# Kernel tuning notes

Hardware: AMD Instinct MI355X
Metric: run time of the kernel (lower is better)

The kernel has to match this reference:

```python
import jax, jax.numpy as jnp
import numpy as np

NSAMPLE = 3  # three_nn default
EPS = 1e-10
CLAMP = 10.0


def setup_inputs() -> dict:
    key = jax.random.key(0)
    k1, k2, k3 = jax.random.split(key, 3)
    B, C, N = 4, 3, 8192
    pos1 = jax.random.normal(k1, (B, C, N), dtype=jnp.float32)
    pos2 = jax.random.normal(k2, (B, C, N), dtype=jnp.float32)
    flow1 = jax.random.normal(k3, (B, C, N), dtype=jnp.float32) * 0.1
    return {"pos1": pos1, "pos2": pos2, "flow1": flow1}


def reference(pos1, pos2, flow1):
    # pos1, flow1: [B,3,N1]; pos2: [B,3,N2]
    pos1_to_2 = pos1 + flow1                       # warped source points [B,3,N1]
    q = jnp.transpose(pos2, (0, 2, 1))             # queries  [B,N2,3]
    k = jnp.transpose(pos1_to_2, (0, 2, 1))        # database [B,N1,3]

    # brute-force 3-NN: squared distances [B,N2,N1]
    d2 = (jnp.sum(q * q, axis=-1, keepdims=True)
          - 2.0 * jnp.einsum('bqc,bnc->bqn', q, k)
          + jnp.sum(k * k, axis=-1)[:, None, :])
    _, knn_idx = jax.lax.top_k(-d2, NSAMPLE)       # [B,N2,NSAMPLE] into N1

    # gather neighbor coords: [B,N2,NSAMPLE,3]
    grouped_pts = jax.vmap(lambda pts, ii: pts[ii])(k, knn_idx)
    diff = grouped_pts - q[:, :, None, :]
    dist = jnp.maximum(jnp.linalg.norm(diff, axis=-1), EPS)  # [B,N2,NSAMPLE]
    inv = 1.0 / dist
    weight = inv / jnp.sum(inv, axis=-1, keepdims=True)      # [B,N2,NSAMPLE]

    # gather neighbor flows and do inverse-distance-weighted average
    flow_t = jnp.transpose(flow1, (0, 2, 1))                 # [B,N1,3]
    grouped_flow = jax.vmap(lambda f, ii: f[ii])(flow_t, knn_idx)  # [B,N2,NSAMPLE,3]
    flow2 = jnp.sum(weight[..., None] * grouped_flow, axis=2)      # [B,N2,3]

    warped = pos2 - jnp.transpose(flow2, (0, 2, 1))          # [B,3,N2]
    return jnp.clip(warped, -CLAMP, CLAMP)
```

## Files before the change

### kernel.cpp

```cpp
#include <hip/hip_runtime.h>
#include <math.h>


#define BB 4
#define NN 8192
#define BBNN (BB * NN)
#define NC 30
#define NCELLS (NC * NC * NC)
#define NCT (BB * NCELLS)
#define GRID_R 3.3f
#define GRID_INVH (1.0f / 0.22f)
#define D3_THR (0.44f * 0.44f * 0.999f)
#define EPB 1024
#define SB 106
#define NZ4 ((NCT + 108 + 4) / 4)
#define ST_PART 0x40000000u
#define ST_DONE 0x80000000u
#define ST_VAL 0x3FFFFFFFu

typedef unsigned long long u64;

__device__ __forceinline__ int cell_of(float x) {
  int c = (int)floorf((x + GRID_R) * GRID_INVH);
  return min(max(c, 0), NC - 1);
}

__device__ __forceinline__ void merge3(u64& a0, u64& a1, u64& a2,
                                       u64 b0, u64 b1, u64 b2) {
  const u64 lo0 = a0 < b0 ? a0 : b0;
  const u64 hi0 = a0 < b0 ? b0 : a0;
  const u64 lo1 = a1 < b1 ? a1 : b1;
  const u64 lo2 = a2 < b2 ? a2 : b2;
  const u64 o1 = hi0 < lo1 ? hi0 : lo1;
  const u64 t = hi0 < lo1 ? lo1 : hi0;
  a0 = lo0;
  a1 = o1;
  a2 = t < lo2 ? t : lo2;
}

__device__ __forceinline__ void insert3(u64& s0, u64& s1, u64& s2, u64 key) {
  const bool c0 = key < s0;
  const bool c1 = key < s1;
  const bool c2 = key < s2;
  s2 = c1 ? s1 : (c2 ? key : s2);
  s1 = c0 ? s0 : (c1 ? key : s1);
  s0 = c0 ? key : s0;
}

__device__ __forceinline__ void wave_merge3(u64& s0, u64& s1, u64& s2) {
#pragma unroll
  for (int mask = 32; mask >= 1; mask >>= 1) {
    const u64 b0 = __shfl_xor(s0, mask, 64);
    const u64 b1 = __shfl_xor(s1, mask, 64);
    const u64 b2 = __shfl_xor(s2, mask, 64);
    merge3(s0, s1, s2, b0, b1, b2);
  }
}

__device__ __forceinline__ void cand1(const float4& a, float qx, float qy,
                                      float qz, u64& s0, u64& s1, u64& s2) {
  const float dx = a.x - qx, dy = a.y - qy, dz = a.z - qz;
  const float d2 = fmaf(dx, dx, fmaf(dy, dy, dz * dz));
  insert3(s0, s1, s2,
          ((u64)__float_as_uint(d2) << 32) | (unsigned)__float_as_uint(a.w));
}

__device__ __forceinline__ void idw_out(int b, int qn, float qx, float qy,
                                        float qz, u64 s0, u64 s1, u64 s2,
                                        const float* __restrict__ P1,
                                        const float* __restrict__ F1,
                                        float* __restrict__ out) {
  const int idxs[3] = {(int)(unsigned)s0 & (NN - 1),
                       (int)(unsigned)s1 & (NN - 1),
                       (int)(unsigned)s2 & (NN - 1)};
  float w[3], gfx[3], gfy[3], gfz[3];
  float wsumv = 0.0f;
#pragma unroll
  for (int r = 0; r < 3; ++r) {
    const int idx = idxs[r];
    const float fx = F1[idx], fy = F1[NN + idx], fz = F1[2 * NN + idx];
    const float kx = P1[idx] + fx;
    const float ky = P1[NN + idx] + fy;
    const float kz = P1[2 * NN + idx] + fz;
    const float dx = kx - qx, dy = ky - qy, dz = kz - qz;
    float d = sqrtf(dx * dx + dy * dy + dz * dz);
    d = fmaxf(d, 1e-10f);
    const float inv = 1.0f / d;
    w[r] = inv; wsumv += inv;
    gfx[r] = fx; gfy[r] = fy; gfz[r] = fz;
  }
  const float invw = 1.0f / wsumv;
  float ox = 0.0f, oy = 0.0f, oz = 0.0f;
#pragma unroll
  for (int r = 0; r < 3; ++r) {
    const float ww = w[r] * invw;
    ox = fmaf(ww, gfx[r], ox);
    oy = fmaf(ww, gfy[r], oy);
    oz = fmaf(ww, gfz[r], oz);
  }
  ox = qx - ox; oy = qy - oy; oz = qz - oz;
  ox = fminf(fmaxf(ox, -10.0f), 10.0f);
  oy = fminf(fmaxf(oy, -10.0f), 10.0f);
  oz = fminf(fmaxf(oz, -10.0f), 10.0f);
  float* o = out + (size_t)b * 3 * NN;
  o[qn] = ox;
  o[NN + qn] = oy;
  o[2 * NN + qn] = oz;
}

__global__ __launch_bounds__(256) void k_zero(int4* __restrict__ p) {
  const int i = blockIdx.x * 256 + threadIdx.x;
  if (i < NZ4) p[i] = make_int4(0, 0, 0, 0);
}

__global__ __launch_bounds__(256) void k_count(const float* __restrict__ p1,
                                               const float* __restrict__ f1,
                                               int* __restrict__ counts) {
  const int gid = blockIdx.x * 256 + threadIdx.x;
  const int b = gid >> 13, n = gid & (NN - 1);
  const float* P = p1 + (size_t)b * 3 * NN;
  const float* F = f1 + (size_t)b * 3 * NN;
  const float x = P[n] + F[n];
  const float y = P[NN + n] + F[NN + n];
  const float z = P[2 * NN + n] + F[2 * NN + n];
  const int cid = (cell_of(z) * NC + cell_of(y)) * NC + cell_of(x);
  atomicAdd(&counts[b * NCELLS + cid], 1);
}

__global__ __launch_bounds__(256) void k_scan(int* __restrict__ counts,
                                              int* __restrict__ offs,
                                              unsigned* __restrict__ scanst) {
  __shared__ int wsums[4];
  __shared__ int sbase;
  const int tid = threadIdx.x, lane = tid & 63, wav = tid >> 6;
  const int bid = blockIdx.x;
  const int c = bid * EPB + tid * 4;
  int4 v = make_int4(0, 0, 0, 0);
  if (c < NCT) {
    v = *reinterpret_cast<const int4*>(counts + c);
    *reinterpret_cast<int4*>(counts + c) = make_int4(0, 0, 0, 0);
  }
  const int sum4 = v.x + v.y + v.z + v.w;
  int incl = sum4;
  for (int off = 1; off < 64; off <<= 1) {
    const int t = __shfl_up(incl, off, 64);
    incl += (lane >= off) ? t : 0;
  }
  if (lane == 63) wsums[wav] = incl;
  __syncthreads();
  int wbase = 0;
#pragma unroll
  for (int w = 0; w < 4; ++w) wbase += (w < wav) ? wsums[w] : 0;
  const int btot = wsums[0] + wsums[1] + wsums[2] + wsums[3];

  if (wav == 0) {
    if (lane == 0) atomicExch(&scanst[bid], ST_PART | (unsigned)btot);
    int base = 0;
    int j0 = bid;
    while (j0 > 0) {
      const int j = j0 - 64 + lane;
      unsigned s;
      if (j >= 0) {
        do { s = atomicAdd(&scanst[j], 0u); } while (s == 0u);
      } else {
        s = ST_DONE;
      }
      const u64 dball = __ballot((s & ST_DONE) != 0);
      int val;
      if (dball) {
        const int hi = 63 - __clzll(dball);
        val = (lane >= hi) ? (int)(s & ST_VAL) : 0;
      } else {
        val = (int)(s & ST_VAL);
      }
      for (int off = 32; off >= 1; off >>= 1) val += __shfl_down(val, off, 64);
      base += __shfl(val, 0, 64);
      if (dball) break;
      j0 -= 64;
    }
    if (lane == 0) {
      atomicExch(&scanst[bid], ST_DONE | (unsigned)(base + btot));
      sbase = base;
    }
  }
  __syncthreads();
  const int excl = sbase + wbase + incl - sum4;
  if (c < NCT) {
    int4 e;
    e.x = excl;
    e.y = excl + v.x;
    e.z = e.y + v.y;
    e.w = e.z + v.z;
    *reinterpret_cast<int4*>(offs + c) = e;
  }
  if (bid == SB - 1 && tid == 0) offs[NCT] = BBNN;
}

__global__ __launch_bounds__(256) void k_scat(const float* __restrict__ p1,
                                              const float* __restrict__ f1,
                                              int* __restrict__ counts,
                                              const int* __restrict__ offs,
                                              float4* __restrict__ csr) {
  const int gid = blockIdx.x * 256 + threadIdx.x;
  const int b = gid >> 13, n = gid & (NN - 1);
  const float* P = p1 + (size_t)b * 3 * NN;
  const float* F = f1 + (size_t)b * 3 * NN;
  const float x = P[n] + F[n];
  const float y = P[NN + n] + F[NN + n];
  const float z = P[2 * NN + n] + F[2 * NN + n];
  const int cid = (cell_of(z) * NC + cell_of(y)) * NC + cell_of(x);
  const int g = b * NCELLS + cid;
  const int rank = atomicAdd(&counts[g], 1);
  csr[offs[g] + rank] = make_float4(x, y, z, __int_as_float(n));
}

__device__ __forceinline__ void scan_col(int st, int en,
                                         const float4* __restrict__ csr,
                                         float qx, float qy, float qz,
                                         u64& s0, u64& s1, u64& s2) {
  int j = st;
  for (; j + 4 <= en; j += 4) {
    const float4 a = csr[j];
    const float4 b = csr[j + 1];
    const float4 c = csr[j + 2];
    const float4 d = csr[j + 3];
    cand1(a, qx, qy, qz, s0, s1, s2);
    cand1(b, qx, qy, qz, s0, s1, s2);
    cand1(c, qx, qy, qz, s0, s1, s2);
    cand1(d, qx, qy, qz, s0, s1, s2);
  }
  for (; j < en; ++j) {
    const float4 a = csr[j];
    cand1(a, qx, qy, qz, s0, s1, s2);
  }
}

__global__ __launch_bounds__(256) void k_query(const float* __restrict__ p1,
                                               const float* __restrict__ p2,
                                               const float* __restrict__ f1,
                                               const int* __restrict__ offs,
                                               const float4* __restrict__ csr,
                                               float* __restrict__ out,
                                               int* __restrict__ fbcnt,
                                               int* __restrict__ fbq) {
  const int gtid = blockIdx.x * 256 + threadIdx.x;
  const int qid = gtid >> 5;
  const int r = gtid & 31;
  const int b = qid >> 13;
  const int qn = qid & (NN - 1);
  const float* P1 = p1 + (size_t)b * 3 * NN;
  const float* P2 = p2 + (size_t)b * 3 * NN;
  const float* F1 = f1 + (size_t)b * 3 * NN;

  const float qx = P2[qn], qy = P2[NN + qn], qz = P2[2 * NN + qn];
  const bool oor = !(fabsf(qx) < GRID_R && fabsf(qy) < GRID_R && fabsf(qz) < GRID_R);

  u64 s0 = ~0ULL, s1 = ~0ULL, s2 = ~0ULL;

  if (!oor && r < 25) {
    const int qcx = cell_of(qx), qcy = cell_of(qy), qcz = cell_of(qz);
    const int gxl = max(qcx - 2, 0);
    const int span = min(qcx + 2, NC - 1) - gxl + 1;
    const int dzi = (r * 205) >> 10;
    const int gz = qcz + dzi - 2;
    const int gy = qcy + (r - dzi * 5) - 2;
    if (((unsigned)gz < NC) & ((unsigned)gy < NC)) {
      const int ia = b * NCELLS + (gz * NC + gy) * NC + gxl;
      const int st = offs[ia];
      const int en = offs[ia + span];
      scan_col(st, en, csr, qx, qy, qz, s0, s1, s2);
    }
  }

#pragma unroll
  for (int mask = 1; mask <= 16; mask <<= 1) {
    const u64 b0 = __shfl_xor(s0, mask, 64);
    const u64 b1 = __shfl_xor(s1, mask, 64);
    const u64 b2 = __shfl_xor(s2, mask, 64);
    merge3(s0, s1, s2, b0, b1, b2);
  }

  if (r == 0) {
    const float d3 = __uint_as_float((unsigned)(s2 >> 32));
    const bool ok = !oor && (d3 <= D3_THR);
    if (!ok) {
      const int slot = atomicAdd(&fbcnt[b], 1);
      fbq[b * NN + slot] = qn;
    } else {
      idw_out(b, qn, qx, qy, qz, s0, s1, s2, P1, F1, out);
    }
  }
}

__global__ __launch_bounds__(256) void k_fallback(const float* __restrict__ p1,
                                                  const float* __restrict__ p2,
                                                  const float* __restrict__ f1,
                                                  const int* __restrict__ fbcnt,
                                                  const int* __restrict__ fbq,
                                                  float* __restrict__ out) {
  __shared__ u64 redA[4][3];
  __shared__ u64 redC[4][3];
  const int b = blockIdx.y;
  const int nfb = fbcnt[b];
  const int tid = threadIdx.x, lane = tid & 63, wav = tid >> 6;
  const float* P1 = p1 + (size_t)b * 3 * NN;
  const float* P2 = p2 + (size_t)b * 3 * NN;
  const float* F1 = f1 + (size_t)b * 3 * NN;
  const int* q = fbq + b * NN;

  for (int base = blockIdx.x * 2; base < nfb; base += gridDim.x * 2) {
    const bool v1 = base + 1 < nfb;
    const int qn0 = q[base] & (NN - 1);
    const int qn1 = (v1 ? q[base + 1] : q[base]) & (NN - 1);
    const float q0x = P2[qn0], q0y = P2[NN + qn0], q0z = P2[2 * NN + qn0];
    const float q1x = P2[qn1], q1y = P2[NN + qn1], q1z = P2[2 * NN + qn1];

    u64 a0 = ~0ULL, a1 = ~0ULL, a2 = ~0ULL;
    u64 c0 = ~0ULL, c1 = ~0ULL, c2 = ~0ULL;

    for (int g0 = 0; g0 < NN; g0 += 1024) {
      const int g = g0 + tid;
      float xs[4], ys[4], zs[4];
#pragma unroll
      for (int k = 0; k < 4; ++k) {
        const int gg = g + k * 256;
        xs[k] = P1[gg] + F1[gg];
        ys[k] = P1[NN + gg] + F1[NN + gg];
        zs[k] = P1[2 * NN + gg] + F1[2 * NN + gg];
      }
#pragma unroll
      for (int k = 0; k < 4; ++k) {
        const unsigned gg = (unsigned)(g + k * 256);
        {
          const float dx = xs[k] - q0x, dy = ys[k] - q0y, dz = zs[k] - q0z;
          const float d2 = fmaf(dx, dx, fmaf(dy, dy, dz * dz));
          insert3(a0, a1, a2, ((u64)__float_as_uint(d2) << 32) | gg);
        }
        {
          const float dx = xs[k] - q1x, dy = ys[k] - q1y, dz = zs[k] - q1z;
          const float d2 = fmaf(dx, dx, fmaf(dy, dy, dz * dz));
          insert3(c0, c1, c2, ((u64)__float_as_uint(d2) << 32) | gg);
        }
      }
    }

    wave_merge3(a0, a1, a2);
    wave_merge3(c0, c1, c2);
    if (lane == 0) {
      redA[wav][0] = a0; redA[wav][1] = a1; redA[wav][2] = a2;
      redC[wav][0] = c0; redC[wav][1] = c1; redC[wav][2] = c2;
    }
    __syncthreads();
    if (tid == 0) {
      u64 m0 = redA[0][0], m1 = redA[0][1], m2 = redA[0][2];
#pragma unroll
      for (int w = 1; w < 4; ++w) merge3(m0, m1, m2, redA[w][0], redA[w][1], redA[w][2]);
      idw_out(b, qn0, q0x, q0y, q0z, m0, m1, m2, P1, F1, out);
    }
    if (tid == 1 && v1) {
      u64 m0 = redC[0][0], m1 = redC[0][1], m2 = redC[0][2];
#pragma unroll
      for (int w = 1; w < 4; ++w) merge3(m0, m1, m2, redC[w][0], redC[w][1], redC[w][2]);
      idw_out(b, qn1, q1x, q1y, q1z, m0, m1, m2, P1, F1, out);
    }
    __syncthreads();
  }
}

extern "C" void kernel_launch(void* const* d_in, const int* in_sizes, int n_in,
                              void* d_out, int out_size, void* d_ws, size_t ws_size,
                              hipStream_t stream) {
  const float* pos1 = (const float*)d_in[0];
  const float* pos2 = (const float*)d_in[1];
  const float* flow1 = (const float*)d_in[2];
  float* out = (float*)d_out;

  char* ws = (char*)d_ws;
  int* counts = (int*)ws;
  unsigned* scanst = (unsigned*)(counts + NCT);
  int* fbcnt = (int*)(counts + NCT + 108);
  size_t offs_off = (size_t)(NCT + 112) * 4;
  int* offs = (int*)(ws + offs_off);
  size_t fbq_off = (offs_off + ((size_t)NCT + 1) * 4 + 15) & ~(size_t)15;
  int* fbq = (int*)(ws + fbq_off);
  size_t csr_off = (fbq_off + (size_t)BBNN * 4 + 15) & ~(size_t)15;
  float4* csr = (float4*)(ws + csr_off);

  k_zero<<<dim3((NZ4 + 255) / 256), dim3(256), 0, stream>>>((int4*)counts);
  k_count<<<dim3(BBNN / 256), dim3(256), 0, stream>>>(pos1, flow1, counts);
  k_scan<<<dim3(SB), dim3(256), 0, stream>>>(counts, offs, scanst);
  k_scat<<<dim3(BBNN / 256), dim3(256), 0, stream>>>(pos1, flow1, counts, offs, csr);
  k_query<<<dim3(BBNN * 32 / 256), dim3(256), 0, stream>>>(pos1, pos2, flow1, offs,
                                                           csr, out, fbcnt, fbq);
  k_fallback<<<dim3(128, BB), dim3(256), 0, stream>>>(pos1, pos2, flow1, fbcnt, fbq, out);
}
```

Measured before the change: 71.05 us.

## Fuse brute-force fallback into query kernel via wave-level inline scan

Removes the separate fallback kernel and its atomic queue. Queries whose grid search fails the distance check are now handled inside the query kernel: a ballot finds the failing half-waves, and the whole 64-lane wave brute-forces all N points for each one. This saves a kernel launch and the queue traffic. The cost is that any wave holding a failing query stalls on an 8192-point scan, which may create tail imbalance if such queries are common.

```diff
diff --git a/kernel.cpp b/kernel.cpp
--- a/kernel.cpp
+++ b/kernel.cpp
@@ -13,7 +13,7 @@
 #define D3_THR (0.44f * 0.44f * 0.999f)
 #define EPB 1024
 #define SB 106
-#define NZ4 ((NCT + 108 + 4) / 4)
+#define NZ4 ((NCT + 108) / 4)
 #define ST_PART 0x40000000u
 #define ST_DONE 0x80000000u
 #define ST_VAL 0x3FFFFFFFu
@@ -45,16 +45,6 @@
   s2 = c1 ? s1 : (c2 ? key : s2);
   s1 = c0 ? s0 : (c1 ? key : s1);
   s0 = c0 ? key : s0;
-}
-
-__device__ __forceinline__ void wave_merge3(u64& s0, u64& s1, u64& s2) {
-#pragma unroll
-  for (int mask = 32; mask >= 1; mask >>= 1) {
-    const u64 b0 = __shfl_xor(s0, mask, 64);
-    const u64 b1 = __shfl_xor(s1, mask, 64);
-    const u64 b2 = __shfl_xor(s2, mask, 64);
-    merge3(s0, s1, s2, b0, b1, b2);
-  }
 }
 
 __device__ __forceinline__ void cand1(const float4& a, float qx, float qy,
@@ -240,10 +230,10 @@
                                                const float* __restrict__ f1,
                                                const int* __restrict__ offs,
                                                const float4* __restrict__ csr,
-                                               float* __restrict__ out,
-                                               int* __restrict__ fbcnt,
-                                               int* __restrict__ fbq) {
-  const int gtid = blockIdx.x * 256 + threadIdx.x;
+                                               float* __restrict__ out) {
+  const int tid = threadIdx.x;
+  const int lane = tid & 63;
+  const int gtid = blockIdx.x * 256 + tid;
   const int qid = gtid >> 5;
   const int r = gtid & 31;
   const int b = qid >> 13;
@@ -280,90 +270,39 @@
     merge3(s0, s1, s2, b0, b1, b2);
   }
 
-  if (r == 0) {
-    const float d3 = __uint_as_float((unsigned)(s2 >> 32));
-    const bool ok = !oor && (d3 <= D3_THR);
-    if (!ok) {
-      const int slot = atomicAdd(&fbcnt[b], 1);
-      fbq[b * NN + slot] = qn;
-    } else {
-      idw_out(b, qn, qx, qy, qz, s0, s1, s2, P1, F1, out);
+  const float d3 = __uint_as_float((unsigned)(s2 >> 32));
+  const bool ok = !oor && (d3 <= D3_THR);
+
+  if (r == 0 && ok) idw_out(b, qn, qx, qy, qz, s0, s1, s2, P1, F1, out);
+
+  const u64 bal = __ballot((r == 0) && !ok);
+  if (bal != 0) {
+#pragma unroll
+    for (int q = 0; q < 2; ++q) {
+      if (!((bal >> (32 * q)) & 1ULL)) continue;
+      const int fqn = __shfl(qn, 32 * q, 64);
+      const float fqx = __shfl(qx, 32 * q, 64);
+      const float fqy = __shfl(qy, 32 * q, 64);
+      const float fqz = __shfl(qz, 32 * q, 64);
+      u64 a0 = ~0ULL, a1 = ~0ULL, a2 = ~0ULL;
+      for (int t = 0; t < NN / 64; ++t) {
+        const int g = t * 64 + lane;
+        const float x = P1[g] + F1[g];
+        const float y = P1[NN + g] + F1[NN + g];
+        const float z = P1[2 * NN + g] + F1[2 * NN + g];
+        const float dx = x - fqx, dy = y - fqy, dz = z - fqz;
+        const float d2 = fmaf(dx, dx, fmaf(dy, dy, dz * dz));
+        insert3(a0, a1, a2, ((u64)__float_as_uint(d2) << 32) | (unsigned)g);
+      }
+#pragma unroll
+      for (int mask = 32; mask >= 1; mask >>= 1) {
+        const u64 b0 = __shfl_xor(a0, mask, 64);
+        const u64 b1 = __shfl_xor(a1, mask, 64);
+        const u64 b2 = __shfl_xor(a2, mask, 64);
+        merge3(a0, a1, a2, b0, b1, b2);
+      }
+      if (lane == 0) idw_out(b, fqn, fqx, fqy, fqz, a0, a1, a2, P1, F1, out);
     }
-  }
-}
-
-__global__ __launch_bounds__(256) void k_fallback(const float* __restrict__ p1,
-                                                  const float* __restrict__ p2,
-                                                  const float* __restrict__ f1,
-                                                  const int* __restrict__ fbcnt,
-                                                  const int* __restrict__ fbq,
-                                                  float* __restrict__ out) {
-  __shared__ u64 redA[4][3];
-  __shared__ u64 redC[4][3];
-  const int b = blockIdx.y;
-  const int nfb = fbcnt[b];
-  const int tid = threadIdx.x, lane = tid & 63, wav = tid >> 6;
-  const float* P1 = p1 + (size_t)b * 3 * NN;
-  const float* P2 = p2 + (size_t)b * 3 * NN;
-  const float* F1 = f1 + (size_t)b * 3 * NN;
-  const int* q = fbq + b * NN;
-
-  for (int base = blockIdx.x * 2; base < nfb; base += gridDim.x * 2) {
-    const bool v1 = base + 1 < nfb;
-    const int qn0 = q[base] & (NN - 1);
-    const int qn1 = (v1 ? q[base + 1] : q[base]) & (NN - 1);
-    const float q0x = P2[qn0], q0y = P2[NN + qn0], q0z = P2[2 * NN + qn0];
-    const float q1x = P2[qn1], q1y = P2[NN + qn1], q1z = P2[2 * NN + qn1];
-
-    u64 a0 = ~0ULL, a1 = ~0ULL, a2 = ~0ULL;
-    u64 c0 = ~0ULL, c1 = ~0ULL, c2 = ~0ULL;
-
-    for (int g0 = 0; g0 < NN; g0 += 1024) {
-      const int g = g0 + tid;
-      float xs[4], ys[4], zs[4];
-#pragma unroll
-      for (int k = 0; k < 4; ++k) {
-        const int gg = g + k * 256;
-        xs[k] = P1[gg] + F1[gg];
-        ys[k] = P1[NN + gg] + F1[NN + gg];
-        zs[k] = P1[2 * NN + gg] + F1[2 * NN + gg];
-      }
-#pragma unroll
-      for (int k = 0; k < 4; ++k) {
-        const unsigned gg = (unsigned)(g + k * 256);
-        {
-          const float dx = xs[k] - q0x, dy = ys[k] - q0y, dz = zs[k] - q0z;
-          const float d2 = fmaf(dx, dx, fmaf(dy, dy, dz * dz));
-          insert3(a0, a1, a2, ((u64)__float_as_uint(d2) << 32) | gg);
-        }
-        {
-          const float dx = xs[k] - q1x, dy = ys[k] - q1y, dz = zs[k] - q1z;
-          const float d2 = fmaf(dx, dx, fmaf(dy, dy, dz * dz));
-          insert3(c0, c1, c2, ((u64)__float_as_uint(d2) << 32) | gg);
-        }
-      }
-    }
-
-    wave_merge3(a0, a1, a2);
-    wave_merge3(c0, c1, c2);
-    if (lane == 0) {
-      redA[wav][0] = a0; redA[wav][1] = a1; redA[wav][2] = a2;
-      redC[wav][0] = c0; redC[wav][1] = c1; redC[wav][2] = c2;
-    }
-    __syncthreads();
-    if (tid == 0) {
-      u64 m0 = redA[0][0], m1 = redA[0][1], m2 = redA[0][2];
-#pragma unroll
-      for (int w = 1; w < 4; ++w) merge3(m0, m1, m2, redA[w][0], redA[w][1], redA[w][2]);
-      idw_out(b, qn0, q0x, q0y, q0z, m0, m1, m2, P1, F1, out);
-    }
-    if (tid == 1 && v1) {
-      u64 m0 = redC[0][0], m1 = redC[0][1], m2 = redC[0][2];
-#pragma unroll
-      for (int w = 1; w < 4; ++w) merge3(m0, m1, m2, redC[w][0], redC[w][1], redC[w][2]);
-      idw_out(b, qn1, q1x, q1y, q1z, m0, m1, m2, P1, F1, out);
-    }
-    __syncthreads();
   }
 }
 
@@ -378,12 +317,9 @@
   char* ws = (char*)d_ws;
   int* counts = (int*)ws;
   unsigned* scanst = (unsigned*)(counts + NCT);
-  int* fbcnt = (int*)(counts + NCT + 108);
-  size_t offs_off = (size_t)(NCT + 112) * 4;
+  size_t offs_off = (size_t)(NCT + 108) * 4;
   int* offs = (int*)(ws + offs_off);
-  size_t fbq_off = (offs_off + ((size_t)NCT + 1) * 4 + 15) & ~(size_t)15;
-  int* fbq = (int*)(ws + fbq_off);
-  size_t csr_off = (fbq_off + (size_t)BBNN * 4 + 15) & ~(size_t)15;
+  size_t csr_off = (offs_off + ((size_t)NCT + 1) * 4 + 15) & ~(size_t)15;
   float4* csr = (float4*)(ws + csr_off);
 
   k_zero<<<dim3((NZ4 + 255) / 256), dim3(256), 0, stream>>>((int4*)counts);
@@ -391,6 +327,5 @@
   k_scan<<<dim3(SB), dim3(256), 0, stream>>>(counts, offs, scanst);
   k_scat<<<dim3(BBNN / 256), dim3(256), 0, stream>>>(pos1, flow1, counts, offs, csr);
   k_query<<<dim3(BBNN * 32 / 256), dim3(256), 0, stream>>>(pos1, pos2, flow1, offs,
-                                                           csr, out, fbcnt, fbq);
-  k_fallback<<<dim3(128, BB), dim3(256), 0, stream>>>(pos1, pos2, flow1, fbcnt, fbq, out);
-}
+                                                           csr, out);
+}
```

New measurement: 86.36 us. 1.22x slower.
